# Performance work log

Hardware: AMD Instinct MI355X
Metric: run time of the kernel (lower is better)

The kernel has to match this reference:

```python
import jax, jax.numpy as jnp
import numpy as np

NUM_BINS = 512
NUM_HEADS = 8
CHANNELS = 512
FFN_HIDDEN = 1024
BN_EPS = 1e-5


def setup_inputs() -> dict:
    key = jax.random.key(0)
    ks = jax.random.split(key, 8)
    B, C, N = 32, CHANNELS, 512
    Fh = FFN_HIDDEN
    inp = {
        "x": jax.random.normal(ks[0], (B, C, N), dtype=jnp.float32),
        "qkv_w": jax.random.normal(ks[1], (3 * C, C), dtype=jnp.float32) * 0.02,
        "qkv_b": jnp.zeros((3 * C,), jnp.float32),
        "out_w": jax.random.normal(ks[2], (C, C), dtype=jnp.float32) * 0.02,
        "out_b": jnp.zeros((C,), jnp.float32),
        "rel_pos_emb": jax.random.normal(ks[3], (2 * NUM_BINS - 1, NUM_HEADS), dtype=jnp.float32) * 0.02,
        "bn1_g": jnp.ones((C,), jnp.float32),
        "bn1_b": jnp.zeros((C,), jnp.float32),
        "bn1_m": jnp.zeros((C,), jnp.float32),
        "bn1_v": jnp.ones((C,), jnp.float32),
        "ffn1_w": jax.random.normal(ks[4], (Fh, C), dtype=jnp.float32) * 0.02,
        "ffn1_b": jnp.zeros((Fh,), jnp.float32),
        "ffn2_w": jax.random.normal(ks[5], (C, Fh), dtype=jnp.float32) * 0.02,
        "ffn2_b": jnp.zeros((C,), jnp.float32),
        "bn2_g": jnp.ones((C,), jnp.float32),
        "bn2_b": jnp.zeros((C,), jnp.float32),
        "bn2_m": jnp.zeros((C,), jnp.float32),
        "bn2_v": jnp.ones((C,), jnp.float32),
    }
    return inp


def _pw_conv(w, b, x):
    # 1x1 Conv1d == per-position linear: w [O, C], x [B, C, N] -> [B, O, N]
    return jnp.einsum('oc,bcn->bon', w, x) + b[None, :, None]


def _bn_eval(x, g, b, m, v):
    # BatchNorm1d in eval mode over channel dim of [B, C, N]
    inv = jax.lax.rsqrt(v + BN_EPS)
    return (x - m[None, :, None]) * (g * inv)[None, :, None] + b[None, :, None]


def reference(x, qkv_w, qkv_b, out_w, out_b, rel_pos_emb,
              bn1_g, bn1_b, bn1_m, bn1_v,
              ffn1_w, ffn1_b, ffn2_w, ffn2_b,
              bn2_g, bn2_b, bn2_m, bn2_v):
    B, C, N = x.shape
    H = NUM_HEADS
    Dh = C // H
    scale = Dh ** (-0.5)

    residual = x
    qkv = _pw_conv(qkv_w, qkv_b, x)                      # [B, 3C, N]
    q, k, v = jnp.split(qkv, 3, axis=1)
    # view(B, H, Dh, N).transpose(-1, -2) -> [B, H, N, Dh]
    q = jnp.swapaxes(q.reshape(B, H, Dh, N), -1, -2)
    k = jnp.swapaxes(k.reshape(B, H, Dh, N), -1, -2)
    v = jnp.swapaxes(v.reshape(B, H, Dh, N), -1, -2)

    attn = jnp.einsum('bhnd,bhmd->bhnm', q, k) * scale   # [B, H, N, N]

    # relative position bias, gathered from the table
    pos_idx = jnp.arange(N)[None, :] - jnp.arange(N)[:, None]
    pos_idx = jnp.clip(pos_idx + NUM_BINS - 1, 0, 2 * NUM_BINS - 2)
    bias = rel_pos_emb[pos_idx]                          # [N, N, H]
    attn = attn + jnp.transpose(bias, (2, 0, 1))[None]   # [1, H, N, N]

    attn = jax.nn.softmax(attn, axis=-1)
    out = jnp.einsum('bhnm,bhmd->bhnd', attn, v)         # [B, H, N, Dh]
    out = jnp.swapaxes(out, -1, -2).reshape(B, C, N)
    out = _pw_conv(out_w, out_b, out)

    h = _bn_eval(out + residual, bn1_g, bn1_b, bn1_m, bn1_v)

    f = _pw_conv(ffn1_w, ffn1_b, h)
    f = jax.nn.gelu(f, approximate=False)
    f = _pw_conv(ffn2_w, ffn2_b, f)

    return _bn_eval(f + h, bn2_g, bn2_b, bn2_m, bn2_v)
```

## Files before the change

### kernel.cpp

```cpp
#include <hip/hip_runtime.h>
#include <cstddef>
#include <cstdint>

constexpr int B_ = 32;
constexpr int C_ = 512;
constexpr int N_ = 512;
constexpr int H_ = 8;
constexpr int FH_ = 1024;
constexpr float BN_EPS_ = 1e-5f;
constexpr float LOG2E_ = 1.44269504088896f;

typedef __attribute__((ext_vector_type(8))) short bf16x8;
typedef __attribute__((ext_vector_type(4))) short s16x4;
typedef __attribute__((ext_vector_type(4))) float f32x4;

enum { EPI_QKV = 0, EPI_BN1 = 1, EPI_GELU = 2, EPI_BN2 = 3 };

__device__ inline void gload_lds16(const void* g, void* l) {
    __builtin_amdgcn_global_load_lds(
        (const __attribute__((address_space(1))) void*)g,
        (__attribute__((address_space(3))) void*)l, 16, 0, 0);
}

__device__ inline short f2bf(float f) {
    union { float f; uint32_t u; } v; v.f = f;
    uint32_t r = v.u + 0x7fffu + ((v.u >> 16) & 1u);
    return (short)(r >> 16);
}

__device__ inline float bf2f(short s) {
    union { uint32_t u; float f; } v;
    v.u = ((uint32_t)(uint16_t)s) << 16;
    return v.f;
}

__device__ inline uint32_t cvt_pk_bf16(float lo, float hi) {
    uint32_t r;
    asm("v_cvt_pk_bf16_f32 %0, %1, %2" : "=v"(r) : "v"(lo), "v"(hi));
    return r;
}

__global__ __launch_bounds__(256) void cvt_weights(
    const float* __restrict__ s0, const float* __restrict__ s1,
    const float* __restrict__ s2, const float* __restrict__ s3,
    short* __restrict__ d)
{
    int i = blockIdx.x * 256 + threadIdx.x;
    const float* src;
    int local;
    if (i < 196608)      { src = s0; local = i; }
    else if (i < 262144) { src = s1; local = i - 196608; }
    else if (i < 393216) { src = s2; local = i - 262144; }
    else                 { src = s3; local = i - 393216; }
    f32x4 v = *(const f32x4*)&src[(size_t)local * 4];
    s16x4 o;
    o[0] = f2bf(v[0]); o[1] = f2bf(v[1]); o[2] = f2bf(v[2]); o[3] = f2bf(v[3]);
    *(s16x4*)&d[(size_t)i * 4] = o;
}

__global__ __launch_bounds__(256) void transpose_x(const float* __restrict__ x,
                                                   short* __restrict__ xT)
{
    __shared__ __align__(16) float s[64][65];
    const int b = blockIdx.z, c0 = blockIdx.x * 64, n0 = blockIdx.y * 64;
    const int t = threadIdx.x;
    const float* xb = x + ((size_t)b * C_ + c0) * N_ + n0;
    {
        int nl = t & 63, cl = t >> 6;
#pragma unroll
        for (int i = 0; i < 16; ++i)
            s[cl + i * 4][nl] = xb[(size_t)(cl + i * 4) * N_ + nl];
    }
    __syncthreads();
    short* xTb = xT + ((size_t)b * N_ + n0) * C_ + c0;
    {
        int cl = t & 63, nl = t >> 6;
#pragma unroll
        for (int i = 0; i < 16; ++i)
            xTb[(size_t)(nl + i * 4) * C_ + cl] = f2bf(s[cl][nl + i * 4]);
    }
}

template <int EPI, int KD, int OSTR, int OB, int NB>
__global__ __launch_bounds__(256) void gemm_mfma(
    const short* __restrict__ A, const short* __restrict__ W,
    const float* __restrict__ bias,
    short* __restrict__ Yb, short* __restrict__ Yv, float* __restrict__ Yf,
    const short* __restrict__ resb,
    const float* __restrict__ g, const float* __restrict__ bt,
    const float* __restrict__ mn, const float* __restrict__ vr)
{
    constexpr int NWG = OB * NB * B_;
    constexpr int CPX = NWG / 8;
    const int bid = blockIdx.x;
    const int swz = (bid & 7) * CPX + (bid >> 3);
    const int ob  = swz % OB;
    const int rst = swz / OB;
    const int b   = rst / NB;
    const int o0  = ob * 128;
    const int n0  = (rst % NB) * 128;
    const short* Ab = A + (size_t)b * 512 * KD;

    __shared__ __align__(16) short As[3][128 * 32];
    __shared__ __align__(16) short Bs[3][128 * 32];

    const int t = threadIdx.x;
    const int lane = t & 63, w = t >> 6;
    const int l15 = lane & 15, lg = lane >> 4;
    const int wr = w >> 1, wc = w & 1;

    const f32x4 zero4 = {0.f, 0.f, 0.f, 0.f};
    f32x4 acc[4][4];
#pragma unroll
    for (int i = 0; i < 4; ++i)
#pragma unroll
        for (int j = 0; j < 4; ++j) acc[i][j] = zero4;

    const int r0 = t >> 2;
    const int kb = (((t & 3) ^ ((t >> 3) & 3)) * 8);

    constexpr int Kt = KD / 32;

#define GSTAGE(bufi, kk0)                                                        \
    do {                                                                         \
        gload_lds16(Ab + (size_t)(n0 + r0) * KD + (kk0) + kb,      &As[bufi][w * 512]);        \
        gload_lds16(Ab + (size_t)(n0 + r0 + 64) * KD + (kk0) + kb, &As[bufi][w * 512 + 2048]); \
        gload_lds16(W  + (size_t)(o0 + r0) * KD + (kk0) + kb,      &Bs[bufi][w * 512]);        \
        gload_lds16(W  + (size_t)(o0 + r0 + 64) * KD + (kk0) + kb, &Bs[bufi][w * 512 + 2048]); \
    } while (0)

    GSTAGE(0, 0);
    GSTAGE(1, 32);

    const int rsw = (lg ^ ((l15 >> 1) & 3)) * 8;

#pragma unroll
    for (int k = 0; k < Kt; ++k) {
        if (k == Kt - 1) asm volatile("s_waitcnt vmcnt(0)" ::: "memory");
        else             asm volatile("s_waitcnt vmcnt(4)" ::: "memory");
        __builtin_amdgcn_s_barrier();
        __builtin_amdgcn_sched_barrier(0);
        if (k + 2 < Kt) GSTAGE((k + 2) % 3, (k + 2) * 32);

        const int u = k % 3;
        bf16x8 af[4], bf[4];
#pragma unroll
        for (int mi = 0; mi < 4; ++mi)
            af[mi] = *(const bf16x8*)&As[u][(wr * 64 + mi * 16 + l15) * 32 + rsw];
#pragma unroll
        for (int ni = 0; ni < 4; ++ni)
            bf[ni] = *(const bf16x8*)&Bs[u][(wc * 64 + ni * 16 + l15) * 32 + rsw];
        __builtin_amdgcn_s_setprio(1);
#pragma unroll
        for (int mi = 0; mi < 4; ++mi)
#pragma unroll
            for (int ni = 0; ni < 4; ++ni)
                acc[mi][ni] = __builtin_amdgcn_mfma_f32_16x16x32_bf16(
                    af[mi], bf[ni], acc[mi][ni], 0, 0, 0);
        __builtin_amdgcn_s_setprio(0);
    }
#undef GSTAGE

#pragma unroll
    for (int mi = 0; mi < 4; ++mi) {
        const int nb2 = n0 + wr * 64 + mi * 16 + lg * 4;
#pragma unroll
        for (int ni = 0; ni < 4; ++ni) {
            const int o = o0 + wc * 64 + ni * 16 + l15;
            const float bv = bias[o];
            f32x4 v = acc[mi][ni];
            if constexpr (EPI == EPI_QKV) {
                if (o0 < 1024) {
#pragma unroll
                    for (int r = 0; r < 4; ++r)
                        Yb[((size_t)b * 512 + nb2 + r) * 1024 + o] = f2bf(v[r] + bv);
                } else {
                    s16x4 pk;
#pragma unroll
                    for (int r = 0; r < 4; ++r) pk[r] = f2bf(v[r] + bv);
                    *(s16x4*)&Yv[((size_t)b * 512 + (o - 1024)) * 512 + nb2] = pk;
                }
            } else if constexpr (EPI == EPI_BN1) {
                const float sc = g[o] * rsqrtf(vr[o] + BN_EPS_);
                const float sh = bt[o] - mn[o] * sc;
#pragma unroll
                for (int r = 0; r < 4; ++r) {
                    float rr = bf2f(resb[((size_t)b * 512 + nb2 + r) * 512 + o]);
                    float val = (v[r] + bv + rr) * sc + sh;
                    Yb[((size_t)b * 512 + nb2 + r) * 512 + o] = f2bf(val);
                }
            } else if constexpr (EPI == EPI_GELU) {
#pragma unroll
                for (int r = 0; r < 4; ++r) {
                    float val = v[r] + bv;
                    val = 0.5f * val * (1.0f + erff(val * 0.70710678118654752f));
                    Yb[((size_t)b * 512 + nb2 + r) * OSTR + o] = f2bf(val);
                }
            } else {
                const float sc = g[o] * rsqrtf(vr[o] + BN_EPS_);
                const float sh = bt[o] - mn[o] * sc;
                f32x4 ov;
#pragma unroll
                for (int r = 0; r < 4; ++r) {
                    float hres = bf2f(resb[((size_t)b * 512 + nb2 + r) * 512 + o]);
                    ov[r] = (v[r] + bv + hres) * sc + sh;
                }
                *(f32x4*)&Yf[((size_t)b * 512 + o) * 512 + nb2] = ov;
            }
        }
    }
}

__global__ __launch_bounds__(512) void attn_mfma(
    const short* __restrict__ qkT, const short* __restrict__ vT,
    const float* __restrict__ rel, short* __restrict__ attnT)
{
    const int id = blockIdx.x;
    const int h  = id & 7;
    const int n0 = ((id >> 3) & 3) * 128;
    const int b  = id >> 5;
    const int t  = threadIdx.x;
    const int lane = t & 63, w = t >> 6;
    const int l15 = lane & 15, lg = lane >> 4;

    __shared__ __align__(16) short Ks[2][64 * 64];
    __shared__ __align__(16) short Vs[2][64 * 64];
    __shared__ __align__(16) short Ps[8 * 16 * 64];
    __shared__ __align__(16) float relh[1024];

    const short* qb = qkT + (size_t)b * 512 * 1024;
    const short* vb = vT + (size_t)b * 512 * 512;

    for (int i = t; i < 1023; i += 512) relh[i] = rel[i * H_ + h] * LOG2E_;

    const int qr = w * 16 + l15;
    const short* qrow = qb + (size_t)(n0 + qr) * 1024 + h * 64;
    bf16x8 aq[2];
    aq[0] = *(const bf16x8*)&qrow[lg * 8];
    aq[1] = *(const bf16x8*)&qrow[32 + lg * 8];

#define KSTAGE(bufi, m0s)                                                        \
    do {                                                                         \
        {                                                                        \
            int fl_ = t * 8;                                                     \
            int r_ = fl_ >> 6;                                                   \
            int blk_ = (fl_ >> 3) & 7;                                           \
            int d_ = ((blk_ ^ (r_ & 7)) << 3);                                   \
            gload_lds16(qb + (size_t)((m0s) + r_) * 1024 + 512 + h * 64 + d_,    \
                        &Ks[bufi][w * 512]);                                     \
        }                                                                        \
        {                                                                        \
            int fl_ = t * 8;                                                     \
            int dr_ = fl_ >> 6;                                                  \
            int blk_ = (fl_ >> 3) & 7;                                           \
            int m_ = ((blk_ ^ (dr_ & 7)) << 3);                                  \
            gload_lds16(vb + (size_t)(h * 64 + dr_) * 512 + (m0s) + m_,          \
                        &Vs[bufi][w * 512]);                                     \
        }                                                                        \
    } while (0)

    KSTAGE(0, 0);
    __syncthreads();

    const f32x4 zero4 = {0.f, 0.f, 0.f, 0.f};
    f32x4 acc_o[4];
#pragma unroll
    for (int dj = 0; dj < 4; ++dj) acc_o[dj] = zero4;

    float rmax = -3e38f, rsum = 0.f;
    const int qglob = n0 + qr;

    int cur = 0;
    for (int tile = 0; tile < 8; ++tile) {
        const int m0 = tile * 64;
        if (tile < 7) KSTAGE(cur ^ 1, m0 + 64);

        f32x4 s4[4];
#pragma unroll
        for (int mi = 0; mi < 4; ++mi) s4[mi] = zero4;
#pragma unroll
        for (int kk = 0; kk < 2; ++kk) {
#pragma unroll
            for (int mi = 0; mi < 4; ++mi) {
                int mr = mi * 16 + l15;
                bf16x8 bk = *(const bf16x8*)&Ks[cur][mr * 64 + (((kk * 4 + lg) ^ (mr & 7)) << 3)];
                s4[mi] = __builtin_amdgcn_mfma_f32_16x16x32_bf16(bk, aq[kk], s4[mi], 0, 0, 0);
            }
        }

        const int ib = m0 + lg * 4 - qglob + 511;
        float tmax = -3e38f;
#pragma unroll
        for (int mi = 0; mi < 4; ++mi)
#pragma unroll
            for (int r = 0; r < 4; ++r) {
                float sv = s4[mi][r] * (0.125f * LOG2E_) + relh[ib + mi * 16 + r];
                s4[mi][r] = sv;
                tmax = fmaxf(tmax, sv);
            }
        tmax = fmaxf(tmax, __shfl_xor(tmax, 16));
        tmax = fmaxf(tmax, __shfl_xor(tmax, 32));

        if (!__all(tmax <= rmax + 8.f)) {
            float nm = fmaxf(rmax, tmax);
            float sc = __builtin_amdgcn_exp2f(rmax - nm);
            rmax = nm;
            rsum *= sc;
            float scl[4];
#pragma unroll
            for (int r = 0; r < 4; ++r)
                scl[r] = __shfl(sc, (lane & 48) | (lg * 4 + r));
#pragma unroll
            for (int dj = 0; dj < 4; ++dj)
#pragma unroll
                for (int r = 0; r < 4; ++r) acc_o[dj][r] *= scl[r];
        }

        float ts = 0.f;
#pragma unroll
        for (int mi = 0; mi < 4; ++mi)
#pragma unroll
            for (int r = 0; r < 4; ++r) {
                float p = __builtin_amdgcn_exp2f(s4[mi][r] - rmax);
                s4[mi][r] = p;
                ts += p;
            }
        ts += __shfl_xor(ts, 16);
        ts += __shfl_xor(ts, 32);
        rsum += ts;

#pragma unroll
        for (int mi = 0; mi < 4; ++mi) {
            uint32_t w01 = cvt_pk_bf16(s4[mi][0], s4[mi][1]);
            uint32_t w23 = cvt_pk_bf16(s4[mi][2], s4[mi][3]);
            int blk = mi * 2 + (lg >> 1);
            int idx = w * 1024 + l15 * 64 + ((blk ^ (l15 & 7)) << 3) + ((lg & 1) << 2);
            *(uint2*)&Ps[idx] = make_uint2(w01, w23);
        }

#pragma unroll
        for (int kk = 0; kk < 2; ++kk) {
            bf16x8 ap = *(const bf16x8*)&Ps[w * 1024 + l15 * 64 + (((kk * 4 + lg) ^ (l15 & 7)) << 3)];
#pragma unroll
            for (int dj = 0; dj < 4; ++dj) {
                int dr = dj * 16 + l15;
                bf16x8 bv = *(const bf16x8*)&Vs[cur][dr * 64 + (((kk * 4 + lg) ^ (dr & 7)) << 3)];
                acc_o[dj] = __builtin_amdgcn_mfma_f32_16x16x32_bf16(ap, bv, acc_o[dj], 0, 0, 0);
            }
        }
        __syncthreads();
        cur ^= 1;
    }
#undef KSTAGE

    float inv = 1.f / rsum;
    float invr[4];
#pragma unroll
    for (int r = 0; r < 4; ++r)
        invr[r] = __shfl(inv, (lane & 48) | (lg * 4 + r));

    short* ob = attnT + (size_t)b * 512 * 512;
#pragma unroll
    for (int dj = 0; dj < 4; ++dj)
#pragma unroll
        for (int reg = 0; reg < 4; ++reg) {
            int nglob = n0 + w * 16 + lg * 4 + reg;
            ob[(size_t)nglob * 512 + h * 64 + dj * 16 + l15] =
                f2bf(acc_o[dj][reg] * invr[reg]);
        }
}

extern "C" void kernel_launch(void* const* d_in, const int* in_sizes, int n_in,
                              void* d_out, int out_size, void* d_ws, size_t ws_size,
                              hipStream_t stream)
{
    const float* x      = (const float*)d_in[0];
    const float* qkv_w  = (const float*)d_in[1];
    const float* qkv_b  = (const float*)d_in[2];
    const float* out_w  = (const float*)d_in[3];
    const float* out_b  = (const float*)d_in[4];
    const float* rel    = (const float*)d_in[5];
    const float* bn1_g  = (const float*)d_in[6];
    const float* bn1_b  = (const float*)d_in[7];
    const float* bn1_m  = (const float*)d_in[8];
    const float* bn1_v  = (const float*)d_in[9];
    const float* ffn1_w = (const float*)d_in[10];
    const float* ffn1_b = (const float*)d_in[11];
    const float* ffn2_w = (const float*)d_in[12];
    const float* ffn2_b = (const float*)d_in[13];
    const float* bn2_g  = (const float*)d_in[14];
    const float* bn2_b  = (const float*)d_in[15];
    const float* bn2_m  = (const float*)d_in[16];
    const float* bn2_v  = (const float*)d_in[17];

    float* out = (float*)d_out;
    short* ws  = (short*)d_ws;

    size_t off = 0;
    short* qkvw_bf = ws + off; off += (size_t)1536 * 512;
    short* outw_bf = ws + off; off += (size_t)512 * 512;
    short* f1w_bf  = ws + off; off += (size_t)1024 * 512;
    short* f2w_bf  = ws + off; off += (size_t)512 * 1024;
    short* xT      = ws + off; off += (size_t)B_ * 512 * 512;
    short* qkT     = ws + off; off += (size_t)B_ * 512 * 1024;
    short* vTb     = ws + off; off += (size_t)B_ * 512 * 512;
    short* attnT   = ws + off; off += (size_t)B_ * 512 * 512;
    short* h_bf    = ws + off; off += (size_t)B_ * 512 * 512;
    short* f1_bf   = ws + off; off += (size_t)B_ * 512 * 1024;

    const dim3 blk(256);
    const dim3 blk512(512);

    cvt_weights<<<dim3(524288 / 256), blk, 0, stream>>>(qkv_w, out_w, ffn1_w, ffn2_w, qkvw_bf);

    transpose_x<<<dim3(8, 8, B_), blk, 0, stream>>>(x, xT);

    gemm_mfma<EPI_QKV, 512, 1024, 12, 4><<<dim3(1536), blk, 0, stream>>>(
        xT, qkvw_bf, qkv_b, qkT, vTb, nullptr, nullptr, nullptr, nullptr, nullptr, nullptr);

    attn_mfma<<<dim3(1024), blk512, 0, stream>>>(qkT, vTb, rel, attnT);

    gemm_mfma<EPI_BN1, 512, 512, 4, 4><<<dim3(512), blk, 0, stream>>>(
        attnT, outw_bf, out_b, h_bf, nullptr, nullptr, xT, bn1_g, bn1_b, bn1_m, bn1_v);

    gemm_mfma<EPI_GELU, 512, 1024, 8, 4><<<dim3(1024), blk, 0, stream>>>(
        h_bf, f1w_bf, ffn1_b, f1_bf, nullptr, nullptr, nullptr, nullptr, nullptr, nullptr, nullptr);

    gemm_mfma<EPI_BN2, 1024, 512, 4, 4><<<dim3(512), blk, 0, stream>>>(
        f1_bf, f2w_bf, ffn2_b, nullptr, nullptr, out, h_bf, bn2_g, bn2_b, bn2_m, bn2_v);
}
```

Measured before the change: 170.1 us.

## Load GEMM MFMA fragments directly from global memory, dropping LDS staging

The pointwise-conv GEMM kernel no longer stages A and W tiles through a triple-buffered LDS pipeline with barriers. Each wave now loads its MFMA operand fragments straight from global memory into registers, double-buffered across k-steps, and issues the MFMAs. This removes LDS traffic and barrier synchronization. In exchange, waves sharing a tile no longer share loads, so global/L2 traffic rises, and each lane reads 16-byte pieces scattered across rows, which coalesces poorly.

New measurement: 338.4 us. 98.9% more time.

```diff
diff --git a/kernel.cpp b/kernel.cpp
--- a/kernel.cpp
+++ b/kernel.cpp
@@ -101,9 +101,6 @@
     const int n0  = (rst % NB) * 128;
     const short* Ab = A + (size_t)b * 512 * KD;
 
-    __shared__ __align__(16) short As[3][128 * 32];
-    __shared__ __align__(16) short Bs[3][128 * 32];
-
     const int t = threadIdx.x;
     const int lane = t & 63, w = t >> 6;
     const int l15 = lane & 15, lg = lane >> 4;
@@ -116,50 +113,47 @@
 #pragma unroll
         for (int j = 0; j < 4; ++j) acc[i][j] = zero4;
 
-    const int r0 = t >> 2;
-    const int kb = (((t & 3) ^ ((t >> 3) & 3)) * 8);
+    const short* ar[4];
+    const short* br[4];
+#pragma unroll
+    for (int mi = 0; mi < 4; ++mi) {
+        ar[mi] = Ab + (size_t)(n0 + wr * 64 + mi * 16 + l15) * KD + lg * 8;
+        br[mi] = W  + (size_t)(o0 + wc * 64 + mi * 16 + l15) * KD + lg * 8;
+    }
 
     constexpr int Kt = KD / 32;
 
-#define GSTAGE(bufi, kk0)                                                        \
+    bf16x8 a0[4], b0[4], a1[4], b1[4];
+
+#define LDFRAG(da, db, kk)                                                       \
     do {                                                                         \
-        gload_lds16(Ab + (size_t)(n0 + r0) * KD + (kk0) + kb,      &As[bufi][w * 512]);        \
-        gload_lds16(Ab + (size_t)(n0 + r0 + 64) * KD + (kk0) + kb, &As[bufi][w * 512 + 2048]); \
-        gload_lds16(W  + (size_t)(o0 + r0) * KD + (kk0) + kb,      &Bs[bufi][w * 512]);        \
-        gload_lds16(W  + (size_t)(o0 + r0 + 64) * KD + (kk0) + kb, &Bs[bufi][w * 512 + 2048]); \
+        _Pragma("unroll")                                                        \
+        for (int mi = 0; mi < 4; ++mi) {                                         \
+            da[mi] = *(const bf16x8*)&ar[mi][(kk) * 32];                         \
+            db[mi] = *(const bf16x8*)&br[mi][(kk) * 32];                         \
+        }                                                                        \
     } while (0)
 
-    GSTAGE(0, 0);
-    GSTAGE(1, 32);
-
-    const int rsw = (lg ^ ((l15 >> 1) & 3)) * 8;
-
-#pragma unroll
-    for (int k = 0; k < Kt; ++k) {
-        if (k == Kt - 1) asm volatile("s_waitcnt vmcnt(0)" ::: "memory");
-        else             asm volatile("s_waitcnt vmcnt(4)" ::: "memory");
-        __builtin_amdgcn_s_barrier();
-        __builtin_amdgcn_sched_barrier(0);
-        if (k + 2 < Kt) GSTAGE((k + 2) % 3, (k + 2) * 32);
-
-        const int u = k % 3;
-        bf16x8 af[4], bf[4];
-#pragma unroll
-        for (int mi = 0; mi < 4; ++mi)
-            af[mi] = *(const bf16x8*)&As[u][(wr * 64 + mi * 16 + l15) * 32 + rsw];
-#pragma unroll
-        for (int ni = 0; ni < 4; ++ni)
-            bf[ni] = *(const bf16x8*)&Bs[u][(wc * 64 + ni * 16 + l15) * 32 + rsw];
-        __builtin_amdgcn_s_setprio(1);
-#pragma unroll
-        for (int mi = 0; mi < 4; ++mi)
-#pragma unroll
-            for (int ni = 0; ni < 4; ++ni)
-                acc[mi][ni] = __builtin_amdgcn_mfma_f32_16x16x32_bf16(
-                    af[mi], bf[ni], acc[mi][ni], 0, 0, 0);
-        __builtin_amdgcn_s_setprio(0);
-    }
-#undef GSTAGE
+#define MFMA16(aa, bb)                                                           \
+    do {                                                                         \
+        _Pragma("unroll")                                                        \
+        for (int mi = 0; mi < 4; ++mi)                                           \
+            _Pragma("unroll")                                                    \
+            for (int ni = 0; ni < 4; ++ni)                                       \
+                acc[mi][ni] = __builtin_amdgcn_mfma_f32_16x16x32_bf16(           \
+                    aa[mi], bb[ni], acc[mi][ni], 0, 0, 0);                       \
+    } while (0)
+
+    LDFRAG(a0, b0, 0);
+#pragma unroll
+    for (int k = 0; k < Kt; k += 2) {
+        LDFRAG(a1, b1, k + 1);
+        MFMA16(a0, b0);
+        if (k + 2 < Kt) LDFRAG(a0, b0, k + 2);
+        MFMA16(a1, b1);
+    }
+#undef LDFRAG
+#undef MFMA16
 
 #pragma unroll
     for (int mi = 0; mi < 4; ++mi) {
```
